# Performance work log

Hardware: AMD Instinct MI355X
Metric: run time of the kernel (lower is better)

## Reference

```python
import jax, jax.numpy as jnp
import numpy as np
import math

B, N, DIM, NH, K, PD = 2, 2048, 512, 8, 32, 16
HD = DIM // NH
LN_EPS = 1e-6  # flax LayerNorm default


def _poincare_dist(x, y, c):
    # x, y broadcast to [B, N, N, PD]; returns [B, N, N]
    diff_norm_sq = jnp.sum((x - y) ** 2, axis=-1)
    x_norm_sq = jnp.sum(x ** 2, axis=-1)
    y_norm_sq = jnp.sum(y ** 2, axis=-1)
    den = (1.0 - c * x_norm_sq) * (1.0 - c * y_norm_sq)
    arg = 1.0 + 2.0 * c * diff_norm_sq / jnp.clip(den, 1e-8)
    safe_arg = jnp.maximum(arg, 1.0 + 1e-7)
    return jnp.arccosh(safe_arg) / jnp.sqrt(c)


def _layernorm(x, scale, bias):
    m = jnp.mean(x, axis=-1, keepdims=True)
    v = jnp.var(x, axis=-1, keepdims=True)
    return (x - m) / jnp.sqrt(v + LN_EPS) * scale + bias


def setup_inputs() -> dict:
    key = jax.random.key(0)
    ks = jax.random.split(key, 12)

    def dense(k, din, dout):
        W = jax.random.normal(k, (din, dout), jnp.float32) / np.sqrt(din).astype(np.float32)
        b = jnp.zeros((dout,), jnp.float32)
        return W, b

    inp = {}
    inp["x"] = jax.random.normal(ks[0], (B, N, DIM), jnp.float32)
    # points inside the unit Poincare ball (c=1)
    inp["positions"] = (jax.random.uniform(ks[1], (B, N, PD), jnp.float32) - 0.5) * 0.2
    inp["c"] = jnp.float32(1.0)
    inp["Wq"], inp["bq"] = dense(ks[2], DIM, DIM)
    inp["Wk"], inp["bk"] = dense(ks[3], DIM, DIM)
    inp["Wv"], inp["bv"] = dense(ks[4], DIM, DIM)
    inp["Wo"], inp["bo"] = dense(ks[5], DIM, DIM)
    inp["W1"], inp["b1"] = dense(ks[6], DIM, 4 * DIM)
    inp["W2"], inp["b2"] = dense(ks[7], 4 * DIM, DIM)
    inp["ln1_scale"] = jnp.ones((DIM,), jnp.float32)
    inp["ln1_bias"] = jnp.zeros((DIM,), jnp.float32)
    inp["ln2_scale"] = jnp.ones((DIM,), jnp.float32)
    inp["ln2_bias"] = jnp.zeros((DIM,), jnp.float32)
    inp["log_tau"] = jnp.zeros((1,), jnp.float32)
    inp["attn_scale"] = jnp.ones((1,), jnp.float32)
    return inp


def reference(x, positions, c, Wq, bq, Wk, bk, Wv, bv, Wo, bo,
              W1, b1, W2, b2, ln1_scale, ln1_bias, ln2_scale, ln2_bias,
              log_tau, attn_scale):
    x_res = x
    x_norm = _layernorm(x, ln1_scale, ln1_bias)

    def heads(W, b):
        return (x_norm @ W + b).reshape(B, N, NH, HD).transpose(0, 2, 1, 3)  # [B,H,N,HD]

    q = heads(Wq, bq)
    k = heads(Wk, bk)
    v = heads(Wv, bv)

    # pairwise hyperbolic distances [B,N,N]
    dist_matrix = _poincare_dist(positions[:, None, :, :], positions[:, :, None, :], c)
    _, top_k_indices = jax.lax.top_k(-dist_matrix, K)  # [B,N,K]

    # gather neighbor K/V: out[b,h,i,j,d] = kv[b,h, idx[b,i,j], d]
    gather = jax.vmap(lambda kv_b, idx_b: kv_b[:, idx_b, :])
    k_gathered = gather(k, top_k_indices)  # [B,H,N,K,HD]
    v_gathered = gather(v, top_k_indices)  # [B,H,N,K,HD]

    feature_scores = jnp.einsum('bhid,bhikd->bhik', q, k_gathered) / math.sqrt(HD)
    gathered_dists = jnp.take_along_axis(dist_matrix, top_k_indices, axis=-1)  # [B,N,K]
    geometric_scores = -gathered_dists[:, None, :, :] / jnp.clip(jnp.exp(log_tau), 1e-8)
    attn_scores = attn_scale * jnp.tanh(feature_scores + geometric_scores)
    attn_weights = jax.nn.softmax(attn_scores, axis=-1)

    attn_output = jnp.einsum('bhik,bhikd->bhid', attn_weights, v_gathered)
    attn_output = attn_output.transpose(0, 2, 1, 3).reshape(B, N, DIM)

    x1 = x_res + attn_output @ Wo + bo
    x2_norm = _layernorm(x1, ln2_scale, ln2_bias)
    ffn = jax.nn.gelu(x2_norm @ W1 + b1) @ W2 + b2  # gelu approximate=True (flax default)
    return x1 + ffn
```

## Files before the change

### kernel.cpp

```cpp
#include <hip/hip_runtime.h>
#include <math.h>

#define B_   2
#define N_   2048
#define DIM_ 512
#define NH_  8
#define HD_  64
#define K_   32
#define PD_  16
#define TOK_ (B_*N_)
#define FFN_ 2048
#define QKV_ (3*DIM_)
#define KV_  1024

typedef __bf16 bf16x8 __attribute__((ext_vector_type(8)));
typedef float  f32x4  __attribute__((ext_vector_type(4)));

__device__ __forceinline__ unsigned short f2bf(float f) {
    unsigned int u = __float_as_uint(f);
    u = (u + 0x7fffu + ((u >> 16) & 1u)) >> 16;
    return (unsigned short)u;
}

__device__ __forceinline__ float bflo(unsigned u) { return __uint_as_float(u << 16); }
__device__ __forceinline__ float bfhi(unsigned u) { return __uint_as_float(u & 0xffff0000u); }

__device__ __forceinline__ float gelu_tanh(float x) {
    float x3 = x * x * x;
    return 0.5f * x * (1.f + tanhf(0.7978845608028654f * (x + 0.044715f * x3)));
}

__device__ __forceinline__ float tanh_fast(float x) {
    float e = __expf(2.f * x);
    return 1.f - 2.f / (e + 1.f);
}

__device__ __forceinline__ int lane_mbcnt(unsigned long long m) {
    return __builtin_amdgcn_mbcnt_hi((unsigned)(m >> 32),
           __builtin_amdgcn_mbcnt_lo((unsigned)m, 0));
}

#define GLOAD_LDS16(g, l) __builtin_amdgcn_global_load_lds(                        \
    (const __attribute__((address_space(1))) unsigned int*)(const void*)(g),       \
    (__attribute__((address_space(3))) unsigned int*)(void*)(l), 16, 0, 0)

__global__ void layernorm_kernel(const float* __restrict__ x,
                                 const float* __restrict__ scale,
                                 const float* __restrict__ bias,
                                 unsigned short* __restrict__ y)
{
    int wave = (blockIdx.x * blockDim.x + threadIdx.x) >> 6;
    int lane = threadIdx.x & 63;
    if (wave >= TOK_) return;
    const float* xr = x + (size_t)wave * DIM_;
    float v[8];
    float s = 0.f;
#pragma unroll
    for (int i = 0; i < 8; i++) { v[i] = xr[lane + i*64]; s += v[i]; }
#pragma unroll
    for (int off = 32; off; off >>= 1) s += __shfl_xor(s, off);
    float mean = s * (1.f / DIM_);
    float vs = 0.f;
#pragma unroll
    for (int i = 0; i < 8; i++) { float d = v[i] - mean; vs += d*d; }
#pragma unroll
    for (int off = 32; off; off >>= 1) vs += __shfl_xor(vs, off);
    float inv = rsqrtf(vs * (1.f / DIM_) + 1e-6f);
    unsigned short* yr = y + (size_t)wave * DIM_;
#pragma unroll
    for (int i = 0; i < 8; i++) {
        int c = lane + i*64;
        yr[c] = f2bf((v[i] - mean) * inv * scale[c] + bias[c]);
    }
}

__global__ void prep_kernel(const float* __restrict__ Wq, const float* __restrict__ Wk,
                            const float* __restrict__ Wv, const float* __restrict__ Wo,
                            const float* __restrict__ W1, const float* __restrict__ W2,
                            const float* __restrict__ bq, const float* __restrict__ bk,
                            const float* __restrict__ bv,
                            unsigned short* __restrict__ qkvWt,
                            unsigned short* __restrict__ WoT,
                            unsigned short* __restrict__ W1T,
                            unsigned short* __restrict__ W2T,
                            float* __restrict__ qkv_b,
                            const float* __restrict__ pos,
                            float* __restrict__ pos_sq)
{
    int id = blockIdx.x;
    if (id >= 3079) {
        int i = (id - 3079) * 256 + threadIdx.x;
        if (i < TOK_) {
            const float4* p = (const float4*)(pos + (size_t)i * PD_);
            float s = 0.f;
#pragma unroll
            for (int d = 0; d < 4; d++) {
                float4 q = p[d];
                s += q.x*q.x + q.y*q.y + q.z*q.z + q.w*q.w;
            }
            pos_sq[i] = s;
        }
        return;
    }
    if (id >= 3072) {
        int i = (id - 3072) * 256 + threadIdx.x;
        if (i < DIM_)            qkv_b[i] = bq[i];
        else if (i < 2*DIM_)     qkv_b[i] = bk[i - DIM_];
        else if (i < 3*DIM_)     qkv_b[i] = bv[i - 2*DIM_];
        return;
    }

    const float* W; unsigned short* Wt; int Kd, Nw, nx, t;
    if      (id < 256)  { W = Wq; Wt = qkvWt;               Kd = 512;  Nw = 512;  nx = 16; t = id; }
    else if (id < 512)  { W = Wk; Wt = qkvWt + 512*512;     Kd = 512;  Nw = 512;  nx = 16; t = id - 256; }
    else if (id < 768)  { W = Wv; Wt = qkvWt + 2*512*512;   Kd = 512;  Nw = 512;  nx = 16; t = id - 512; }
    else if (id < 1024) { W = Wo; Wt = WoT;                 Kd = 512;  Nw = 512;  nx = 16; t = id - 768; }
    else if (id < 2048) { W = W1; Wt = W1T;                 Kd = 512;  Nw = 2048; nx = 64; t = id - 1024; }
    else                { W = W2; Wt = W2T;                 Kd = 2048; Nw = 512;  nx = 16; t = id - 2048; }

    __shared__ float tile[32][33];
    int n0 = (t % nx) * 32, k0 = (t / nx) * 32;
    int tx = threadIdx.x & 31, ty = threadIdx.x >> 5;
#pragma unroll
    for (int i = 0; i < 32; i += 8)
        tile[ty + i][tx] = W[(size_t)(k0 + ty + i) * Nw + n0 + tx];
    __syncthreads();
#pragma unroll
    for (int i = 0; i < 32; i += 8)
        Wt[(size_t)(n0 + ty + i) * Kd + k0 + tx] = f2bf(tile[tx][ty + i]);
}

template<int EPI, int BM, int BN>
__global__ __launch_bounds__(256)
void gemm_bf16_kernel(const unsigned short* __restrict__ A,
                      const unsigned short* __restrict__ Bt,
                      const float* __restrict__ bias,
                      const float* __restrict__ res,
                      float* __restrict__ Cf,
                      unsigned short* __restrict__ Cb,
                      int M, int N, int Kd)
{
    constexpr int WM = BM / 2;
    constexpr int WN = BN / 2;
    constexpr int FM = WM / 16;
    constexpr int FN = WN / 16;

    __shared__ unsigned short As[BM*32];
    __shared__ unsigned short Bs[BN*32];

    int t    = threadIdx.x;
    int lane = t & 63;
    int wid  = t >> 6;
    int wm   = wid >> 1, wn = wid & 1;

    int bm0 = blockIdx.y * BM;
    int bn0 = blockIdx.x * BN;

    f32x4 acc[FM][FN] = {};

    int kc    = lane >> 4;
    int rlo   = lane & 15;

    for (int k0 = 0; k0 < Kd; k0 += 32) {
#pragma unroll
        for (int l = 0; l < BM/64; l++) {
            int idx = l*256 + t;
            int row = idx >> 2;
            int gc  = (idx & 3) ^ ((row >> 1) & 3);
            GLOAD_LDS16(A + (size_t)(bm0 + row) * Kd + k0 + gc*8, As + idx*8);
        }
#pragma unroll
        for (int l = 0; l < BN/64; l++) {
            int idx = l*256 + t;
            int row = idx >> 2;
            int gc  = (idx & 3) ^ ((row >> 1) & 3);
            GLOAD_LDS16(Bt + (size_t)(bn0 + row) * Kd + k0 + gc*8, Bs + idx*8);
        }
        __syncthreads();

        bf16x8 af[FM], bf[FN];
#pragma unroll
        for (int mi = 0; mi < FM; mi++) {
            int r = wm*WM + mi*16 + rlo;
            af[mi] = *(const bf16x8*)(As + r*32 + (kc ^ ((r>>1)&3))*8);
        }
#pragma unroll
        for (int ni = 0; ni < FN; ni++) {
            int r = wn*WN + ni*16 + rlo;
            bf[ni] = *(const bf16x8*)(Bs + r*32 + (kc ^ ((r>>1)&3))*8);
        }
#pragma unroll
        for (int mi = 0; mi < FM; mi++)
#pragma unroll
            for (int ni = 0; ni < FN; ni++)
                acc[mi][ni] = __builtin_amdgcn_mfma_f32_16x16x32_bf16(
                    af[mi], bf[ni], acc[mi][ni], 0, 0, 0);
        __syncthreads();
    }

#pragma unroll
    for (int mi = 0; mi < FM; mi++) {
#pragma unroll
        for (int ni = 0; ni < FN; ni++) {
            int col = bn0 + wn*WN + ni*16 + rlo;
            float bv = bias[col];
#pragma unroll
            for (int r = 0; r < 4; r++) {
                int row = bm0 + wm*WM + mi*16 + kc*4 + r;
                float val = acc[mi][ni][r] + bv;
                if (EPI == 1) val += res[(size_t)row * N + col];
                if (EPI == 2) {
                    val = gelu_tanh(val);
                    Cb[(size_t)row * N + col] = f2bf(val);
                } else if (EPI == 3) {
                    if (col < DIM_) Cf[(size_t)row * DIM_ + col] = val;
                    else            Cb[(size_t)row * KV_ + (col - DIM_)] = f2bf(val);
                } else {
                    Cf[(size_t)row * N + col] = val;
                }
            }
        }
    }
}

__global__ __launch_bounds__(256)
void dist_topk_split_kernel(const float* __restrict__ pos, const float* __restrict__ pos_sq,
                            const float* __restrict__ c_ptr,
                            int* __restrict__ topk_idx, float* __restrict__ topk_dist)
{
    __shared__ unsigned long long cand[2][64];

    int wid  = threadIdx.x >> 6;
    int lane = threadIdx.x & 63;
    int rw   = wid >> 1;
    int hw   = wid & 1;
    int bi   = blockIdx.x * 2 + rw;
    int b    = bi >> 11;
    float c  = *c_ptr;
    float inv_sqrt_c = rsqrtf(c);

    const float4* pi4 = (const float4*)(pos + (size_t)bi * PD_);
    float4 p0 = pi4[0], p1 = pi4[1], p2 = pi4[2], p3 = pi4[3];
    float ni = pos_sq[bi];
    float omci = 1.f - c * ni;

    const float* pb  = pos + (size_t)b * N_ * PD_;
    const float* sqb = pos_sq + b * N_;
    int jbase = hw * 1024;

    unsigned rb[16];
#pragma unroll
    for (int tt = 0; tt < 16; tt++) {
        int j = jbase + tt*64 + lane;
        const float4* pj = (const float4*)(pb + (size_t)j * PD_);
        float4 q0 = pj[0], q1 = pj[1], q2 = pj[2], q3 = pj[3];
        float diff =
            (p0.x-q0.x)*(p0.x-q0.x) + (p0.y-q0.y)*(p0.y-q0.y) +
            (p0.z-q0.z)*(p0.z-q0.z) + (p0.w-q0.w)*(p0.w-q0.w) +
            (p1.x-q1.x)*(p1.x-q1.x) + (p1.y-q1.y)*(p1.y-q1.y) +
            (p1.z-q1.z)*(p1.z-q1.z) + (p1.w-q1.w)*(p1.w-q1.w) +
            (p2.x-q2.x)*(p2.x-q2.x) + (p2.y-q2.y)*(p2.y-q2.y) +
            (p2.z-q2.z)*(p2.z-q2.z) + (p2.w-q2.w)*(p2.w-q2.w) +
            (p3.x-q3.x)*(p3.x-q3.x) + (p3.y-q3.y)*(p3.y-q3.y) +
            (p3.z-q3.z)*(p3.z-q3.z) + (p3.w-q3.w)*(p3.w-q3.w);
        float den = fmaxf(omci * (1.f - c * sqb[j]), 1e-8f);
        float arg = fmaxf(1.f + 2.f * c * diff / den, 1.f + 1e-7f);
        rb[tt] = __float_as_uint(arg);
    }

    unsigned T = 0;
    for (int bit = 30; bit >= 0; --bit) {
        unsigned probe = T | (1u << bit);
        int cnt = 0;
#pragma unroll
        for (int tt = 0; tt < 16; tt++)
            cnt += __popcll(__ballot(rb[tt] < probe));
        if (cnt < K_) T = probe;
    }

    int cnt_lt = 0;
#pragma unroll
    for (int tt = 0; tt < 16; tt++)
        cnt_lt += __popcll(__ballot(rb[tt] < T));
    int m = K_ - cnt_lt;

    int ltbase = 0, eqbase = 0;
#pragma unroll
    for (int tt = 0; tt < 16; tt++) {
        bool is_lt = rb[tt] < T;
        bool is_eq = rb[tt] == T;
        unsigned long long mlt = __ballot(is_lt);
        unsigned long long meq = __ballot(is_eq);
        int plt = ltbase + lane_mbcnt(mlt);
        int peq = eqbase + lane_mbcnt(meq);
        unsigned long long key =
            ((unsigned long long)rb[tt] << 32) | (unsigned)(jbase + tt*64 + lane);
        if (is_lt)                 cand[rw][hw*K_ + plt] = key;
        else if (is_eq && peq < m) cand[rw][hw*K_ + cnt_lt + peq] = key;
        ltbase += __popcll(mlt);
        eqbase += __popcll(meq);
    }
    __syncthreads();

    if (hw == 0) {
        unsigned long long mykey = cand[rw][lane];
        int rank = 0;
#pragma unroll 8
        for (int M = 0; M < 64; M++)
            rank += (cand[rw][M] < mykey) ? 1 : 0;
        if (rank < K_) {
            unsigned rbv = (unsigned)(mykey >> 32);
            int      j   = (int)(mykey & 0xffffffffu);
            topk_idx [(size_t)bi * K_ + rank] = j;
            topk_dist[(size_t)bi * K_ + rank] = acoshf(__uint_as_float(rbv)) * inv_sqrt_c;
        }
    }
}

__global__ __launch_bounds__(256)
void attn_kernel(const float* __restrict__ q,
                 const unsigned short* __restrict__ kv,
                 const int* __restrict__ topk_idx, const float* __restrict__ topk_dist,
                 const float* __restrict__ log_tau_p, const float* __restrict__ attn_scale_p,
                 unsigned int* __restrict__ out)
{
    int gw   = (blockIdx.x * blockDim.x + threadIdx.x) >> 6;
    int lane = threadIdx.x & 63;
    if (gw >= B_ * NH_ * N_) return;
    int b = gw / (NH_ * N_);
    int r = gw % (NH_ * N_);
    int h = r / N_;
    int i = r % N_;
    int tok = b * N_ + i;

    float tau    = fmaxf(__expf(*log_tau_p), 1e-8f);
    float ascale = *attn_scale_p;

    const int*   idxp = topk_idx  + (size_t)tok * K_;
    const float* dstp = topk_dist + (size_t)tok * K_;
    int   my_idx  = idxp[lane & 31];
    float my_dist = dstp[lane & 31];

    int jj   = lane >> 1;
    int half = lane & 1;

    const float4* qp = (const float4*)(q + (size_t)tok * DIM_ + h * HD_ + half * 32);
    float4 qv[8];
#pragma unroll
    for (int u = 0; u < 8; u++) qv[u] = qp[u];

    int nb = __shfl(my_idx, jj);
    const uint4* kp = (const uint4*)(kv + (size_t)(b * N_ + nb) * KV_ + h * HD_ + half * 32);
    float dot = 0.f;
#pragma unroll
    for (int u = 0; u < 4; u++) {
        uint4 kw = kp[u];
        dot += qv[2*u].x   * bflo(kw.x) + qv[2*u].y   * bfhi(kw.x)
             + qv[2*u].z   * bflo(kw.y) + qv[2*u].w   * bfhi(kw.y)
             + qv[2*u+1].x * bflo(kw.z) + qv[2*u+1].y * bfhi(kw.z)
             + qv[2*u+1].z * bflo(kw.w) + qv[2*u+1].w * bfhi(kw.w);
    }
    dot += __shfl_xor(dot, 1);

    float fs = dot * 0.125f;
    float gs = -__shfl(my_dist, jj) / tau;
    float s  = ascale * tanh_fast(fs + gs);

    float mx = s;
#pragma unroll
    for (int off = 32; off; off >>= 1) mx = fmaxf(mx, __shfl_xor(mx, off));
    float e  = __expf(s - mx);
    float ec = half ? 0.f : e;
#pragma unroll
    for (int off = 32; off; off >>= 1) ec += __shfl_xor(ec, off);
    float inv = 1.f / ec;

    int dp    = lane & 31;
    int half2 = lane >> 5;
    const unsigned int* vb = (const unsigned int*)(kv + DIM_ + h * HD_) + dp;
    float ax = 0.f, ay = 0.f;
#pragma unroll
    for (int it = 0; it < 16; it++) {
        int t2 = half2 + 2*it;
        float w  = __shfl(e, t2 * 2) * inv;
        int   nj = __shfl(my_idx, t2);
        unsigned vv = vb[(size_t)(b * N_ + nj) * (KV_/2)];
        ax += w * bflo(vv);
        ay += w * bfhi(vv);
    }
    ax += __shfl_xor(ax, 32);
    ay += __shfl_xor(ay, 32);
    if (lane < 32) {
        unsigned pck = ((unsigned)f2bf(ay) << 16) | (unsigned)f2bf(ax);
        out[(size_t)tok * (DIM_/2) + h * (HD_/2) + dp] = pck;
    }
}

extern "C" void kernel_launch(void* const* d_in, const int* in_sizes, int n_in,
                              void* d_out, int out_size, void* d_ws, size_t ws_size,
                              hipStream_t stream)
{
    const float* x          = (const float*)d_in[0];
    const float* positions  = (const float*)d_in[1];
    const float* c_p        = (const float*)d_in[2];
    const float* Wq         = (const float*)d_in[3];
    const float* bq         = (const float*)d_in[4];
    const float* Wk         = (const float*)d_in[5];
    const float* bk         = (const float*)d_in[6];
    const float* Wv         = (const float*)d_in[7];
    const float* bv         = (const float*)d_in[8];
    const float* Wo         = (const float*)d_in[9];
    const float* bo         = (const float*)d_in[10];
    const float* W1         = (const float*)d_in[11];
    const float* b1         = (const float*)d_in[12];
    const float* W2         = (const float*)d_in[13];
    const float* b2         = (const float*)d_in[14];
    const float* ln1_scale  = (const float*)d_in[15];
    const float* ln1_bias   = (const float*)d_in[16];
    const float* ln2_scale  = (const float*)d_in[17];
    const float* ln2_bias   = (const float*)d_in[18];
    const float* log_tau    = (const float*)d_in[19];
    const float* attn_scale = (const float*)d_in[20];

    char* p = (char*)d_ws;
    unsigned short* qkvWt  = (unsigned short*)p; p += (size_t)QKV_ * DIM_ * 2;
    unsigned short* WoT    = (unsigned short*)p; p += (size_t)DIM_ * DIM_ * 2;
    unsigned short* W1T    = (unsigned short*)p; p += (size_t)FFN_ * DIM_ * 2;
    unsigned short* W2T    = (unsigned short*)p; p += (size_t)DIM_ * FFN_ * 2;
    float*          qkv_b  = (float*)p;          p += (size_t)QKV_ * 4;
    unsigned short* xn     = (unsigned short*)p; p += (size_t)TOK_ * DIM_ * 2;
    float*          qf     = (float*)p;          p += (size_t)TOK_ * DIM_ * 4;
    unsigned short* kvb    = (unsigned short*)p; p += (size_t)TOK_ * KV_ * 2;
    unsigned short* attn_o = (unsigned short*)p; p += (size_t)TOK_ * DIM_ * 2;
    float*          x1     = (float*)p;          p += (size_t)TOK_ * DIM_ * 4;
    unsigned short* x2n    = (unsigned short*)p; p += (size_t)TOK_ * DIM_ * 2;
    unsigned short* hbuf   = (unsigned short*)p; p += (size_t)TOK_ * FFN_ * 2;
    float*          pos_sq = (float*)p;          p += (size_t)TOK_ * 4;
    float*          tk_d   = (float*)p;          p += (size_t)TOK_ * K_ * 4;
    int*            tk_i   = (int*)p;            p += (size_t)TOK_ * K_ * 4;

    prep_kernel<<<3095, 256, 0, stream>>>(Wq, Wk, Wv, Wo, W1, W2, bq, bk, bv,
                                          qkvWt, WoT, W1T, W2T, qkv_b,
                                          positions, pos_sq);

    layernorm_kernel<<<TOK_/4, 256, 0, stream>>>(x, ln1_scale, ln1_bias, xn);

    gemm_bf16_kernel<3,128,128><<<dim3(QKV_/128, TOK_/128), 256, 0, stream>>>(
        xn, qkvWt, qkv_b, nullptr, qf, kvb, TOK_, QKV_, DIM_);

    dist_topk_split_kernel<<<TOK_/2, 256, 0, stream>>>(positions, pos_sq, c_p, tk_i, tk_d);

    attn_kernel<<<(B_*NH_*N_)/4, 256, 0, stream>>>(qf, kvb, tk_i, tk_d,
                                                   log_tau, attn_scale,
                                                   (unsigned int*)attn_o);

    gemm_bf16_kernel<1,64,64><<<dim3(DIM_/64, TOK_/64), 256, 0, stream>>>(
        attn_o, WoT, bo, x, x1, nullptr, TOK_, DIM_, DIM_);

    layernorm_kernel<<<TOK_/4, 256, 0, stream>>>(x1, ln2_scale, ln2_bias, x2n);

    gemm_bf16_kernel<2,128,128><<<dim3(FFN_/128, TOK_/128), 256, 0, stream>>>(
        x2n, W1T, b1, nullptr, nullptr, hbuf, TOK_, FFN_, DIM_);

    gemm_bf16_kernel<1,64,64><<<dim3(DIM_/64, TOK_/64), 256, 0, stream>>>(
        hbuf, W2T, b2, x1, (float*)d_out, nullptr, TOK_, DIM_, FFN_);
}
```

Baseline: 273.9 us.

## Fuse prep with layernorm, co-launch QKV GEMM with dist-topk, widen GEMM K-step

Merges weight prep, position prep and the first layernorm into one launch. The QKV GEMM and the distance/top-k search now run as two block ranges of one kernel, so they overlap instead of running back to back. The GEMM K-step grows from 32 to 64 with a new LDS swizzle, halving barrier count per tile at the cost of more shared memory. Distance reads now use a transposed position layout for coalesced loads.

Measured after the change: 396.3 us. +44.7%, slower.

```diff
diff --git a/kernel.cpp b/kernel.cpp
--- a/kernel.cpp
+++ b/kernel.cpp
@@ -44,157 +44,75 @@
     (const __attribute__((address_space(1))) unsigned int*)(const void*)(g),       \
     (__attribute__((address_space(3))) unsigned int*)(void*)(l), 16, 0, 0)
 
-__global__ void layernorm_kernel(const float* __restrict__ x,
-                                 const float* __restrict__ scale,
-                                 const float* __restrict__ bias,
-                                 unsigned short* __restrict__ y)
-{
-    int wave = (blockIdx.x * blockDim.x + threadIdx.x) >> 6;
-    int lane = threadIdx.x & 63;
-    if (wave >= TOK_) return;
-    const float* xr = x + (size_t)wave * DIM_;
-    float v[8];
-    float s = 0.f;
-#pragma unroll
-    for (int i = 0; i < 8; i++) { v[i] = xr[lane + i*64]; s += v[i]; }
-#pragma unroll
-    for (int off = 32; off; off >>= 1) s += __shfl_xor(s, off);
-    float mean = s * (1.f / DIM_);
-    float vs = 0.f;
-#pragma unroll
-    for (int i = 0; i < 8; i++) { float d = v[i] - mean; vs += d*d; }
-#pragma unroll
-    for (int off = 32; off; off >>= 1) vs += __shfl_xor(vs, off);
-    float inv = rsqrtf(vs * (1.f / DIM_) + 1e-6f);
-    unsigned short* yr = y + (size_t)wave * DIM_;
-#pragma unroll
-    for (int i = 0; i < 8; i++) {
-        int c = lane + i*64;
-        yr[c] = f2bf((v[i] - mean) * inv * scale[c] + bias[c]);
-    }
-}
-
-__global__ void prep_kernel(const float* __restrict__ Wq, const float* __restrict__ Wk,
-                            const float* __restrict__ Wv, const float* __restrict__ Wo,
-                            const float* __restrict__ W1, const float* __restrict__ W2,
-                            const float* __restrict__ bq, const float* __restrict__ bk,
-                            const float* __restrict__ bv,
-                            unsigned short* __restrict__ qkvWt,
-                            unsigned short* __restrict__ WoT,
-                            unsigned short* __restrict__ W1T,
-                            unsigned short* __restrict__ W2T,
-                            float* __restrict__ qkv_b,
-                            const float* __restrict__ pos,
-                            float* __restrict__ pos_sq)
-{
-    int id = blockIdx.x;
-    if (id >= 3079) {
-        int i = (id - 3079) * 256 + threadIdx.x;
-        if (i < TOK_) {
-            const float4* p = (const float4*)(pos + (size_t)i * PD_);
-            float s = 0.f;
-#pragma unroll
-            for (int d = 0; d < 4; d++) {
-                float4 q = p[d];
-                s += q.x*q.x + q.y*q.y + q.z*q.z + q.w*q.w;
-            }
-            pos_sq[i] = s;
-        }
-        return;
-    }
-    if (id >= 3072) {
-        int i = (id - 3072) * 256 + threadIdx.x;
-        if (i < DIM_)            qkv_b[i] = bq[i];
-        else if (i < 2*DIM_)     qkv_b[i] = bk[i - DIM_];
-        else if (i < 3*DIM_)     qkv_b[i] = bv[i - 2*DIM_];
-        return;
-    }
-
-    const float* W; unsigned short* Wt; int Kd, Nw, nx, t;
-    if      (id < 256)  { W = Wq; Wt = qkvWt;               Kd = 512;  Nw = 512;  nx = 16; t = id; }
-    else if (id < 512)  { W = Wk; Wt = qkvWt + 512*512;     Kd = 512;  Nw = 512;  nx = 16; t = id - 256; }
-    else if (id < 768)  { W = Wv; Wt = qkvWt + 2*512*512;   Kd = 512;  Nw = 512;  nx = 16; t = id - 512; }
-    else if (id < 1024) { W = Wo; Wt = WoT;                 Kd = 512;  Nw = 512;  nx = 16; t = id - 768; }
-    else if (id < 2048) { W = W1; Wt = W1T;                 Kd = 512;  Nw = 2048; nx = 64; t = id - 1024; }
-    else                { W = W2; Wt = W2T;                 Kd = 2048; Nw = 512;  nx = 16; t = id - 2048; }
-
-    __shared__ float tile[32][33];
-    int n0 = (t % nx) * 32, k0 = (t / nx) * 32;
-    int tx = threadIdx.x & 31, ty = threadIdx.x >> 5;
-#pragma unroll
-    for (int i = 0; i < 32; i += 8)
-        tile[ty + i][tx] = W[(size_t)(k0 + ty + i) * Nw + n0 + tx];
-    __syncthreads();
-#pragma unroll
-    for (int i = 0; i < 32; i += 8)
-        Wt[(size_t)(n0 + ty + i) * Kd + k0 + tx] = f2bf(tile[tx][ty + i]);
-}
-
 template<int EPI, int BM, int BN>
-__global__ __launch_bounds__(256)
-void gemm_bf16_kernel(const unsigned short* __restrict__ A,
+__device__ __forceinline__ void gemm_body(unsigned short* smem, int bx, int by,
+                      const unsigned short* __restrict__ A,
                       const unsigned short* __restrict__ Bt,
                       const float* __restrict__ bias,
                       const float* __restrict__ res,
                       float* __restrict__ Cf,
                       unsigned short* __restrict__ Cb,
-                      int M, int N, int Kd)
+                      int N, int Kd)
 {
     constexpr int WM = BM / 2;
     constexpr int WN = BN / 2;
     constexpr int FM = WM / 16;
     constexpr int FN = WN / 16;
 
-    __shared__ unsigned short As[BM*32];
-    __shared__ unsigned short Bs[BN*32];
+    unsigned short* As_ = smem;
+    unsigned short* Bs_ = smem + BM * 64;
 
     int t    = threadIdx.x;
     int lane = t & 63;
     int wid  = t >> 6;
     int wm   = wid >> 1, wn = wid & 1;
-
-    int bm0 = blockIdx.y * BM;
-    int bn0 = blockIdx.x * BN;
+    int bm0  = by * BM;
+    int bn0  = bx * BN;
+    int quad = lane >> 4;
+    int rlo  = lane & 15;
 
     f32x4 acc[FM][FN] = {};
 
-    int kc    = lane >> 4;
-    int rlo   = lane & 15;
-
-    for (int k0 = 0; k0 < Kd; k0 += 32) {
-#pragma unroll
-        for (int l = 0; l < BM/64; l++) {
+    for (int k0 = 0; k0 < Kd; k0 += 64) {
+#pragma unroll
+        for (int l = 0; l < BM/32; l++) {
             int idx = l*256 + t;
-            int row = idx >> 2;
-            int gc  = (idx & 3) ^ ((row >> 1) & 3);
-            GLOAD_LDS16(A + (size_t)(bm0 + row) * Kd + k0 + gc*8, As + idx*8);
-        }
-#pragma unroll
-        for (int l = 0; l < BN/64; l++) {
+            int r   = idx >> 3;
+            int g   = (idx & 7) ^ (r & 7);
+            GLOAD_LDS16(A + (size_t)(bm0 + r) * Kd + k0 + g*8, As_ + idx*8);
+        }
+#pragma unroll
+        for (int l = 0; l < BN/32; l++) {
             int idx = l*256 + t;
-            int row = idx >> 2;
-            int gc  = (idx & 3) ^ ((row >> 1) & 3);
-            GLOAD_LDS16(Bt + (size_t)(bn0 + row) * Kd + k0 + gc*8, Bs + idx*8);
+            int r   = idx >> 3;
+            int g   = (idx & 7) ^ (r & 7);
+            GLOAD_LDS16(Bt + (size_t)(bn0 + r) * Kd + k0 + g*8, Bs_ + idx*8);
         }
         __syncthreads();
 
-        bf16x8 af[FM], bf[FN];
+        bf16x8 af[FM][2], bfr[FN][2];
 #pragma unroll
         for (int mi = 0; mi < FM; mi++) {
             int r = wm*WM + mi*16 + rlo;
-            af[mi] = *(const bf16x8*)(As + r*32 + (kc ^ ((r>>1)&3))*8);
+#pragma unroll
+            for (int s = 0; s < 2; s++)
+                af[mi][s] = *(const bf16x8*)(As_ + r*64 + ((s*4 + quad) ^ (r & 7))*8);
         }
 #pragma unroll
         for (int ni = 0; ni < FN; ni++) {
             int r = wn*WN + ni*16 + rlo;
-            bf[ni] = *(const bf16x8*)(Bs + r*32 + (kc ^ ((r>>1)&3))*8);
-        }
-#pragma unroll
-        for (int mi = 0; mi < FM; mi++)
-#pragma unroll
-            for (int ni = 0; ni < FN; ni++)
-                acc[mi][ni] = __builtin_amdgcn_mfma_f32_16x16x32_bf16(
-                    af[mi], bf[ni], acc[mi][ni], 0, 0, 0);
+#pragma unroll
+            for (int s = 0; s < 2; s++)
+                bfr[ni][s] = *(const bf16x8*)(Bs_ + r*64 + ((s*4 + quad) ^ (r & 7))*8);
+        }
+#pragma unroll
+        for (int s = 0; s < 2; s++)
+#pragma unroll
+            for (int mi = 0; mi < FM; mi++)
+#pragma unroll
+                for (int ni = 0; ni < FN; ni++)
+                    acc[mi][ni] = __builtin_amdgcn_mfma_f32_16x16x32_bf16(
+                        af[mi][s], bfr[ni][s], acc[mi][ni], 0, 0, 0);
         __syncthreads();
     }
 
@@ -206,7 +124,7 @@
             float bv = bias[col];
 #pragma unroll
             for (int r = 0; r < 4; r++) {
-                int row = bm0 + wm*WM + mi*16 + kc*4 + r;
+                int row = bm0 + wm*WM + mi*16 + quad*4 + r;
                 float val = acc[mi][ni][r] + bv;
                 if (EPI == 1) val += res[(size_t)row * N + col];
                 if (EPI == 2) {
@@ -223,28 +141,50 @@
     }
 }
 
+template<int EPI, int BM, int BN>
 __global__ __launch_bounds__(256)
-void dist_topk_split_kernel(const float* __restrict__ pos, const float* __restrict__ pos_sq,
-                            const float* __restrict__ c_ptr,
-                            int* __restrict__ topk_idx, float* __restrict__ topk_dist)
-{
-    __shared__ unsigned long long cand[2][64];
-
+void gemm_bf16_kernel(const unsigned short* __restrict__ A,
+                      const unsigned short* __restrict__ Bt,
+                      const float* __restrict__ bias,
+                      const float* __restrict__ res,
+                      float* __restrict__ Cf,
+                      unsigned short* __restrict__ Cb,
+                      int N, int Kd)
+{
+    __shared__ __align__(16) unsigned short smem[(BM+BN)*64];
+    gemm_body<EPI,BM,BN>(smem, blockIdx.x, blockIdx.y, A, Bt, bias, res, Cf, Cb, N, Kd);
+}
+
+__device__ __forceinline__ void dist_body(unsigned long long* cand,
+                      int id,
+                      const float* __restrict__ pos,
+                      const float* __restrict__ posT,
+                      const float* __restrict__ pos_sq,
+                      const float* __restrict__ c_ptr,
+                      int* __restrict__ topk_idx, float* __restrict__ topk_dist)
+{
     int wid  = threadIdx.x >> 6;
     int lane = threadIdx.x & 63;
     int rw   = wid >> 1;
     int hw   = wid & 1;
-    int bi   = blockIdx.x * 2 + rw;
+    int bi   = id * 2 + rw;
     int b    = bi >> 11;
     float c  = *c_ptr;
     float inv_sqrt_c = rsqrtf(c);
 
-    const float4* pi4 = (const float4*)(pos + (size_t)bi * PD_);
-    float4 p0 = pi4[0], p1 = pi4[1], p2 = pi4[2], p3 = pi4[3];
+    float pi[16];
+    {
+        const float4* pi4 = (const float4*)(pos + (size_t)bi * PD_);
+        float4 a0 = pi4[0], a1 = pi4[1], a2 = pi4[2], a3 = pi4[3];
+        pi[0]=a0.x; pi[1]=a0.y; pi[2]=a0.z; pi[3]=a0.w;
+        pi[4]=a1.x; pi[5]=a1.y; pi[6]=a1.z; pi[7]=a1.w;
+        pi[8]=a2.x; pi[9]=a2.y; pi[10]=a2.z; pi[11]=a2.w;
+        pi[12]=a3.x; pi[13]=a3.y; pi[14]=a3.z; pi[15]=a3.w;
+    }
     float ni = pos_sq[bi];
     float omci = 1.f - c * ni;
 
-    const float* pb  = pos + (size_t)b * N_ * PD_;
+    const float* pT  = posT + (size_t)b * 16 * N_;
     const float* sqb = pos_sq + b * N_;
     int jbase = hw * 1024;
 
@@ -252,17 +192,12 @@
 #pragma unroll
     for (int tt = 0; tt < 16; tt++) {
         int j = jbase + tt*64 + lane;
-        const float4* pj = (const float4*)(pb + (size_t)j * PD_);
-        float4 q0 = pj[0], q1 = pj[1], q2 = pj[2], q3 = pj[3];
-        float diff =
-            (p0.x-q0.x)*(p0.x-q0.x) + (p0.y-q0.y)*(p0.y-q0.y) +
-            (p0.z-q0.z)*(p0.z-q0.z) + (p0.w-q0.w)*(p0.w-q0.w) +
-            (p1.x-q1.x)*(p1.x-q1.x) + (p1.y-q1.y)*(p1.y-q1.y) +
-            (p1.z-q1.z)*(p1.z-q1.z) + (p1.w-q1.w)*(p1.w-q1.w) +
-            (p2.x-q2.x)*(p2.x-q2.x) + (p2.y-q2.y)*(p2.y-q2.y) +
-            (p2.z-q2.z)*(p2.z-q2.z) + (p2.w-q2.w)*(p2.w-q2.w) +
-            (p3.x-q3.x)*(p3.x-q3.x) + (p3.y-q3.y)*(p3.y-q3.y) +
-            (p3.z-q3.z)*(p3.z-q3.z) + (p3.w-q3.w)*(p3.w-q3.w);
+        float diff = 0.f;
+#pragma unroll
+        for (int d = 0; d < 16; d++) {
+            float dd = pi[d] - pT[d * N_ + j];
+            diff += dd * dd;
+        }
         float den = fmaxf(omci * (1.f - c * sqb[j]), 1e-8f);
         float arg = fmaxf(1.f + 2.f * c * diff / den, 1.f + 1e-7f);
         rb[tt] = __float_as_uint(arg);
@@ -295,25 +230,164 @@
         int peq = eqbase + lane_mbcnt(meq);
         unsigned long long key =
             ((unsigned long long)rb[tt] << 32) | (unsigned)(jbase + tt*64 + lane);
-        if (is_lt)                 cand[rw][hw*K_ + plt] = key;
-        else if (is_eq && peq < m) cand[rw][hw*K_ + cnt_lt + peq] = key;
+        if (is_lt)                 cand[rw*64 + hw*K_ + plt] = key;
+        else if (is_eq && peq < m) cand[rw*64 + hw*K_ + cnt_lt + peq] = key;
         ltbase += __popcll(mlt);
         eqbase += __popcll(meq);
     }
     __syncthreads();
 
     if (hw == 0) {
-        unsigned long long mykey = cand[rw][lane];
+        unsigned long long mykey = cand[rw*64 + lane];
         int rank = 0;
 #pragma unroll 8
         for (int M = 0; M < 64; M++)
-            rank += (cand[rw][M] < mykey) ? 1 : 0;
+            rank += (cand[rw*64 + M] < mykey) ? 1 : 0;
         if (rank < K_) {
             unsigned rbv = (unsigned)(mykey >> 32);
             int      j   = (int)(mykey & 0xffffffffu);
             topk_idx [(size_t)bi * K_ + rank] = j;
             topk_dist[(size_t)bi * K_ + rank] = acoshf(__uint_as_float(rbv)) * inv_sqrt_c;
         }
+    }
+}
+
+__global__ __launch_bounds__(256)
+void qkv_dist_kernel(const unsigned short* __restrict__ xn,
+                     const unsigned short* __restrict__ qkvWt,
+                     const float* __restrict__ qkv_b,
+                     float* __restrict__ qf, unsigned short* __restrict__ kvb,
+                     const float* __restrict__ pos, const float* __restrict__ posT,
+                     const float* __restrict__ pos_sq, const float* __restrict__ c_ptr,
+                     int* __restrict__ tk_i, float* __restrict__ tk_d)
+{
+    __shared__ __align__(16) unsigned short smem[16384];
+    if (blockIdx.x < 384) {
+        gemm_body<3,128,128>(smem, blockIdx.x % 12, blockIdx.x / 12,
+                             xn, qkvWt, qkv_b, nullptr, qf, kvb, QKV_, DIM_);
+    } else {
+        dist_body((unsigned long long*)smem, blockIdx.x - 384,
+                  pos, posT, pos_sq, c_ptr, tk_i, tk_d);
+    }
+}
+
+__global__ void fused_prep_kernel(const float* __restrict__ Wq, const float* __restrict__ Wk,
+                            const float* __restrict__ Wv, const float* __restrict__ Wo,
+                            const float* __restrict__ W1, const float* __restrict__ W2,
+                            const float* __restrict__ bq, const float* __restrict__ bk,
+                            const float* __restrict__ bv,
+                            unsigned short* __restrict__ qkvWt,
+                            unsigned short* __restrict__ WoT,
+                            unsigned short* __restrict__ W1T,
+                            unsigned short* __restrict__ W2T,
+                            float* __restrict__ qkv_b,
+                            const float* __restrict__ pos,
+                            float* __restrict__ pos_sq,
+                            float* __restrict__ posT,
+                            const float* __restrict__ x,
+                            const float* __restrict__ ln1_scale,
+                            const float* __restrict__ ln1_bias,
+                            unsigned short* __restrict__ xn)
+{
+    int id = blockIdx.x;
+    int t  = threadIdx.x;
+
+    if (id >= 3094) {
+        int wave = (id - 3094) * 4 + (t >> 6);
+        int lane = t & 63;
+        const float* xr = x + (size_t)wave * DIM_;
+        float v[8];
+        float s = 0.f;
+#pragma unroll
+        for (int i = 0; i < 8; i++) { v[i] = xr[lane + i*64]; s += v[i]; }
+#pragma unroll
+        for (int off = 32; off; off >>= 1) s += __shfl_xor(s, off);
+        float mean = s * (1.f / DIM_);
+        float vs = 0.f;
+#pragma unroll
+        for (int i = 0; i < 8; i++) { float d = v[i] - mean; vs += d*d; }
+#pragma unroll
+        for (int off = 32; off; off >>= 1) vs += __shfl_xor(vs, off);
+        float inv = rsqrtf(vs * (1.f / DIM_) + 1e-6f);
+        unsigned short* yr = xn + (size_t)wave * DIM_;
+#pragma unroll
+        for (int i = 0; i < 8; i++) {
+            int cc = lane + i*64;
+            yr[cc] = f2bf((v[i] - mean) * inv * ln1_scale[cc] + ln1_bias[cc]);
+        }
+        return;
+    }
+    if (id >= 3078) {
+        int i = (id - 3078) * 256 + t;
+        int b = i >> 11, j = i & (N_ - 1);
+        const float4* p = (const float4*)(pos + (size_t)i * PD_);
+        float4 a0 = p[0], a1 = p[1], a2 = p[2], a3 = p[3];
+        float pv[16] = {a0.x,a0.y,a0.z,a0.w, a1.x,a1.y,a1.z,a1.w,
+                        a2.x,a2.y,a2.z,a2.w, a3.x,a3.y,a3.z,a3.w};
+        float s = 0.f;
+#pragma unroll
+        for (int d = 0; d < 16; d++) s += pv[d]*pv[d];
+        pos_sq[i] = s;
+        float* pT = posT + (size_t)b * 16 * N_;
+#pragma unroll
+        for (int d = 0; d < 16; d++) pT[d * N_ + j] = pv[d];
+        return;
+    }
+    if (id >= 3072) {
+        int i = (id - 3072) * 256 + t;
+        if (i < DIM_)            qkv_b[i] = bq[i];
+        else if (i < 2*DIM_)     qkv_b[i] = bk[i - DIM_];
+        else                     qkv_b[i] = bv[i - 2*DIM_];
+        return;
+    }
+
+    const float* W; unsigned short* Wt; int Kd, Nw, nx, ti;
+    if      (id < 256)  { W = Wq; Wt = qkvWt;               Kd = 512;  Nw = 512;  nx = 16; ti = id; }
+    else if (id < 512)  { W = Wk; Wt = qkvWt + 512*512;     Kd = 512;  Nw = 512;  nx = 16; ti = id - 256; }
+    else if (id < 768)  { W = Wv; Wt = qkvWt + 2*512*512;   Kd = 512;  Nw = 512;  nx = 16; ti = id - 512; }
+    else if (id < 1024) { W = Wo; Wt = WoT;                 Kd = 512;  Nw = 512;  nx = 16; ti = id - 768; }
+    else if (id < 2048) { W = W1; Wt = W1T;                 Kd = 512;  Nw = 2048; nx = 64; ti = id - 1024; }
+    else                { W = W2; Wt = W2T;                 Kd = 2048; Nw = 512;  nx = 16; ti = id - 2048; }
+
+    __shared__ float tile[32][33];
+    int n0 = (ti % nx) * 32, k0 = (ti / nx) * 32;
+    int tx = t & 31, ty = t >> 5;
+#pragma unroll
+    for (int i = 0; i < 32; i += 8)
+        tile[ty + i][tx] = W[(size_t)(k0 + ty + i) * Nw + n0 + tx];
+    __syncthreads();
+#pragma unroll
+    for (int i = 0; i < 32; i += 8)
+        Wt[(size_t)(n0 + ty + i) * Kd + k0 + tx] = f2bf(tile[tx][ty + i]);
+}
+
+__global__ void layernorm_kernel(const float* __restrict__ x,
+                                 const float* __restrict__ scale,
+                                 const float* __restrict__ bias,
+                                 unsigned short* __restrict__ y)
+{
+    int wave = (blockIdx.x * blockDim.x + threadIdx.x) >> 6;
+    int lane = threadIdx.x & 63;
+    if (wave >= TOK_) return;
+    const float* xr = x + (size_t)wave * DIM_;
+    float v[8];
+    float s = 0.f;
+#pragma unroll
+    for (int i = 0; i < 8; i++) { v[i] = xr[lane + i*64]; s += v[i]; }
+#pragma unroll
+    for (int off = 32; off; off >>= 1) s += __shfl_xor(s, off);
+    float mean = s * (1.f / DIM_);
+    float vs = 0.f;
+#pragma unroll
+    for (int i = 0; i < 8; i++) { float d = v[i] - mean; vs += d*d; }
+#pragma unroll
+    for (int off = 32; off; off >>= 1) vs += __shfl_xor(vs, off);
+    float inv = rsqrtf(vs * (1.f / DIM_) + 1e-6f);
+    unsigned short* yr = y + (size_t)wave * DIM_;
+#pragma unroll
+    for (int i = 0; i < 8; i++) {
+        int c = lane + i*64;
+        yr[c] = f2bf((v[i] - mean) * inv * scale[c] + bias[c]);
     }
 }
 
@@ -436,32 +510,31 @@
     unsigned short* x2n    = (unsigned short*)p; p += (size_t)TOK_ * DIM_ * 2;
     unsigned short* hbuf   = (unsigned short*)p; p += (size_t)TOK_ * FFN_ * 2;
     float*          pos_sq = (float*)p;          p += (size_t)TOK_ * 4;
+    float*          posT   = (float*)p;          p += (size_t)B_ * 16 * N_ * 4;
     float*          tk_d   = (float*)p;          p += (size_t)TOK_ * K_ * 4;
     int*            tk_i   = (int*)p;            p += (size_t)TOK_ * K_ * 4;
 
-    prep_kernel<<<3095, 256, 0, stream>>>(Wq, Wk, Wv, Wo, W1, W2, bq, bk, bv,
-                                          qkvWt, WoT, W1T, W2T, qkv_b,
-                                          positions, pos_sq);
-
-    layernorm_kernel<<<TOK_/4, 256, 0, stream>>>(x, ln1_scale, ln1_bias, xn);
-
-    gemm_bf16_kernel<3,128,128><<<dim3(QKV_/128, TOK_/128), 256, 0, stream>>>(
-        xn, qkvWt, qkv_b, nullptr, qf, kvb, TOK_, QKV_, DIM_);
-
-    dist_topk_split_kernel<<<TOK_/2, 256, 0, stream>>>(positions, pos_sq, c_p, tk_i, tk_d);
+    fused_prep_kernel<<<4118, 256, 0, stream>>>(Wq, Wk, Wv, Wo, W1, W2, bq, bk, bv,
+                                                qkvWt, WoT, W1T, W2T, qkv_b,
+                                                positions, pos_sq, posT,
+                                                x, ln1_scale, ln1_bias, xn);
+
+    qkv_dist_kernel<<<384 + TOK_/2, 256, 0, stream>>>(
+        xn, qkvWt, qkv_b, qf, kvb,
+        positions, posT, pos_sq, c_p, tk_i, tk_d);
 
     attn_kernel<<<(B_*NH_*N_)/4, 256, 0, stream>>>(qf, kvb, tk_i, tk_d,
                                                    log_tau, attn_scale,
                                                    (unsigned int*)attn_o);
 
     gemm_bf16_kernel<1,64,64><<<dim3(DIM_/64, TOK_/64), 256, 0, stream>>>(
-        attn_o, WoT, bo, x, x1, nullptr, TOK_, DIM_, DIM_);
+        attn_o, WoT, bo, x, x1, nullptr, DIM_, DIM_);
 
     layernorm_kernel<<<TOK_/4, 256, 0, stream>>>(x1, ln2_scale, ln2_bias, x2n);
 
     gemm_bf16_kernel<2,128,128><<<dim3(FFN_/128, TOK_/128), 256, 0, stream>>>(
-        x2n, W1T, b1, nullptr, nullptr, hbuf, TOK_, FFN_, DIM_);
+        x2n, W1T, b1, nullptr, nullptr, hbuf, FFN_, DIM_);
 
     gemm_bf16_kernel<1,64,64><<<dim3(DIM_/64, TOK_/64), 256, 0, stream>>>(
-        hbuf, W2T, b2, x1, (float*)d_out, nullptr, TOK_, DIM_, FFN_);
-}
+        hbuf, W2T, b2, x1, (float*)d_out, nullptr, DIM_, FFN_);
+}
```
